# Optimization experiments

Hardware: AMD Instinct MI355X
Metric: run time of the kernel (lower is better)

The kernel has to match this reference:

```python
import jax, jax.numpy as jnp
import numpy as np

H = 4          # heads
C = 32         # out_channels per head
NEG_SLOPE = 0.2
N_NODES = 50000
N_EDGES = 600000
F_IN = 128
OUT_DIM = 10
N_GRAPHS = 32


def _gat_params(keys, f_in, scale=0.05):
    hc = H * C
    return dict(
        Wl=jax.random.normal(keys[0], (f_in, hc)) * scale,
        bl=jnp.zeros((hc,)),
        Wr=jax.random.normal(keys[1], (f_in, hc)) * scale,
        br=jnp.zeros((hc,)),
        We=jax.random.normal(keys[2], (1, hc)) * scale,   # lin_edge, bias=False in PyG
        att=jax.random.normal(keys[3], (H, C)) * scale,
        bias=jnp.zeros((hc,)),
    )


def setup_inputs() -> dict:
    key = jax.random.key(0)
    ks = jax.random.split(key, 16)
    x = jax.random.normal(ks[0], (N_NODES, F_IN), dtype=jnp.float32)
    edge_index = jax.random.randint(ks[1], (2, N_EDGES), 0, N_NODES, dtype=jnp.int32)
    edge_weight = jax.random.uniform(ks[2], (N_EDGES, 1), dtype=jnp.float32)
    batch = jnp.sort(jax.random.randint(ks[3], (N_NODES,), 0, N_GRAPHS, dtype=jnp.int32))
    p1 = _gat_params(ks[4:8], F_IN)
    p2 = _gat_params(ks[8:12], H * C)
    fc_W = jax.random.normal(ks[12], (H * C, OUT_DIM)) * 0.05
    fc_b = jnp.zeros((OUT_DIM,))
    return dict(
        x=x, edge_index=edge_index, edge_weight=edge_weight, batch=batch,
        p1_Wl=p1['Wl'], p1_bl=p1['bl'], p1_Wr=p1['Wr'], p1_br=p1['br'],
        p1_We=p1['We'], p1_att=p1['att'], p1_bias=p1['bias'],
        p2_Wl=p2['Wl'], p2_bl=p2['bl'], p2_Wr=p2['Wr'], p2_br=p2['br'],
        p2_We=p2['We'], p2_att=p2['att'], p2_bias=p2['bias'],
        fc_W=fc_W, fc_b=fc_b,
    )


def _add_self_loops(src, dst, eattr, n):
    # PyG fill_value='mean': self-loop attr = mean of incoming edge_attr per node
    loop = jnp.arange(n, dtype=src.dtype)
    cnt = jax.ops.segment_sum(jnp.ones((src.shape[0],), eattr.dtype), dst, num_segments=n)
    loop_attr = jax.ops.segment_sum(eattr, dst, num_segments=n) / jnp.maximum(cnt, 1.0)[:, None]
    return (jnp.concatenate([src, loop]), jnp.concatenate([dst, loop]),
            jnp.concatenate([eattr, loop_attr], axis=0))


def _gatv2_conv(x, src, dst, eattr, Wl, bl, Wr, br, We, att, bias, n):
    x_l = (x @ Wl + bl).reshape(n, H, C)   # source transform
    x_r = (x @ Wr + br).reshape(n, H, C)   # target transform
    e_feat = (eattr @ We).reshape(-1, H, C)
    # per-edge message [E2, H, C]
    m = jax.nn.leaky_relu(x_l[src] + x_r[dst] + e_feat, NEG_SLOPE)
    alpha = jnp.einsum('ehc,hc->eh', m, att)            # [E2, H]
    amax = jax.ops.segment_max(alpha, dst, num_segments=n)
    amax = jnp.where(jnp.isfinite(amax), amax, 0.0)
    ex = jnp.exp(alpha - amax[dst])
    denom = jax.ops.segment_sum(ex, dst, num_segments=n)
    a = ex / (denom[dst] + 1e-16)                       # segment softmax
    out = jax.ops.segment_sum(a[:, :, None] * x_l[src], dst, num_segments=n)
    return out.reshape(n, H * C) + bias


def reference(x, edge_index, edge_weight, batch,
              p1_Wl, p1_bl, p1_Wr, p1_br, p1_We, p1_att, p1_bias,
              p2_Wl, p2_bl, p2_Wr, p2_br, p2_We, p2_att, p2_bias,
              fc_W, fc_b):
    n = x.shape[0]
    src, dst, eattr = _add_self_loops(edge_index[0], edge_index[1], edge_weight, n)
    h = _gatv2_conv(x, src, dst, eattr, p1_Wl, p1_bl, p1_Wr, p1_br, p1_We, p1_att, p1_bias, n)
    h = _gatv2_conv(h, src, dst, eattr, p2_Wl, p2_bl, p2_Wr, p2_br, p2_We, p2_att, p2_bias, n)
    cnt = jax.ops.segment_sum(jnp.ones((n,), h.dtype), batch, num_segments=N_GRAPHS)
    pooled = jax.ops.segment_sum(h, batch, num_segments=N_GRAPHS) / jnp.maximum(cnt, 1.0)[:, None]
    out = pooled @ fc_W + fc_b
    return out, pooled
```

## Files before the change

kernel.cpp:

```cpp
#include <hip/hip_runtime.h>
#include <hip/hip_bf16.h>
#include <cstdint>

static inline int cdiv(int a, int b){ return (a + b - 1) / b; }

typedef __attribute__((ext_vector_type(8))) short short8v;
typedef __attribute__((ext_vector_type(4))) float float4v;
typedef __attribute__((ext_vector_type(2))) float f2;

#define ELLW 48

__device__ inline float bf2f(unsigned short u){ return __uint_as_float(((unsigned)u) << 16); }
__device__ inline unsigned short f2bf(float f){
  unsigned u = __float_as_uint(f);
  u += 0x7fffu + ((u >> 16) & 1u);
  return (unsigned short)(u >> 16);
}
__device__ inline float4 ldbf4(const unsigned short* p){
  ushort4 u = *(const ushort4*)p;
  return make_float4(bf2f(u.x), bf2f(u.y), bf2f(u.z), bf2f(u.w));
}
__device__ inline f2 lo2(float4 v){ f2 r; r.x = v.x; r.y = v.y; return r; }
__device__ inline f2 hi2(float4 v){ f2 r; r.x = v.z; r.y = v.w; return r; }
__device__ inline int sniff16(const unsigned* __restrict__ xw){
  int good = 0;
  #pragma unroll
  for (int j = 0; j < 16; ++j){
    float v = __uint_as_float(xw[j] << 16);
    float a = fabsf(v);
    good += (v == 0.f) || (a >= 6.1e-5f && a <= 64.f);
  }
  return good > 8;
}

struct P16 { const void* p[16]; };
__global__ void k_prep(P16 s, const unsigned* __restrict__ xw,
                       unsigned long long* __restrict__ deg64, float* __restrict__ pool,
                       int pz, int N,
                       unsigned short* __restrict__ Wf, unsigned short* __restrict__ bb,
                       unsigned short* __restrict__ sm){
  int i = blockIdx.x * blockDim.x + threadIdx.x;
  if (i < N) deg64[i] = 0ull;
  if (i < pz) pool[i] = 0.f;
  if (i >= 68106) return;
  const int bf = sniff16(xw);
  auto rd = [&](const void* q, int j) -> unsigned short {
    return bf ? ((const unsigned short*)q)[j] : f2bf(((const float*)q)[j]);
  };
  if (i < 65536){
    int l = i >> 15, r = i & 32767;
    int j = r & 7, n = (r >> 3) & 255, kq = r >> 11;
    int k = kq * 8 + j;
    const void* W = (n < 128) ? (l ? s.p[7] : s.p[0]) : (l ? s.p[9] : s.p[2]);
    Wf[i] = rd(W, k * 128 + (n & 127));
  } else if (i < 66048){
    int i2 = i - 65536;
    int l = i2 >> 8, n = i2 & 255;
    const void* b = (n < 128) ? (l ? s.p[8] : s.p[1]) : (l ? s.p[10] : s.p[3]);
    bb[i2] = rd(b, n & 127);
  } else {
    int j = i - 66048;
    const void* q; int o;
    if      (j < 128){ q = s.p[4];  o = j; }
    else if (j < 256){ q = s.p[5];  o = j - 128; }
    else if (j < 384){ q = s.p[6];  o = j - 256; }
    else if (j < 512){ q = s.p[11]; o = j - 384; }
    else if (j < 640){ q = s.p[12]; o = j - 512; }
    else if (j < 768){ q = s.p[13]; o = j - 640; }
    else if (j < 2048){ q = s.p[14]; o = j - 768; }
    else { q = s.p[15]; o = j - 2048; }
    sm[j] = rd(q, o);
  }
}

__global__ __launch_bounds__(256)
void k_esc(const int* __restrict__ ei, const void* __restrict__ ew,
           const unsigned* __restrict__ xw,
           unsigned long long* __restrict__ deg64, unsigned* __restrict__ eE,
           int E, int P, int N){
  const int bf = sniff16(xw);
  const int part = blockIdx.x & 7;
  const int lo = part * P;
  const int hi = min(lo + P, N);
  const int base = (int)(blockIdx.x >> 3) * 2048;
  const int end = min(base + 2048, E);
  for (int e = base + (int)threadIdx.x; e < end; e += 256){
    int dst = ei[E + e];
    if (dst < lo || dst >= hi) continue;
    int src = ei[e];
    unsigned short w16; float w;
    if (bf){ w16 = ((const unsigned short*)ew)[e]; w = bf2f(w16); }
    else   { w = ((const float*)ew)[e]; w16 = f2bf(w); }
    unsigned long long pk = (1ull << 40) + (unsigned long long)(unsigned)(w * 1048576.0f + 0.5f);
    unsigned long long old = atomicAdd(&deg64[dst], pk);
    int pos = min((int)(old >> 40), ELLW - 1);
    eE[dst * ELLW + pos] = (unsigned)src | ((unsigned)w16 << 16);
  }
}

template<bool ACT_BF_FIXED>
__global__ __launch_bounds__(256)
void k_gemm2(const void* __restrict__ actv, const unsigned* __restrict__ xw,
             const unsigned short* __restrict__ Wf, const unsigned short* __restrict__ bb,
             unsigned short* __restrict__ outL, unsigned short* __restrict__ outR, int nrows){
  __shared__ unsigned short As[64][136];
  __shared__ unsigned short Cs[4][64][40];
  const int abf = ACT_BF_FIXED ? 1 : sniff16(xw);
  const int t = threadIdx.x;
  const int row0 = blockIdx.x * 64;
  for (int c = t; c < 2048; c += 256){
    int row = c >> 5, col4 = (c & 31) * 4;
    int r = row0 + row;
    ushort4 v = make_ushort4(0, 0, 0, 0);
    if (r < nrows){
      if (abf) v = *(const ushort4*)((const unsigned short*)actv + (size_t)r * 128 + col4);
      else {
        float4 f = *(const float4*)((const float*)actv + (size_t)r * 128 + col4);
        v.x = f2bf(f.x); v.y = f2bf(f.y); v.z = f2bf(f.z); v.w = f2bf(f.w);
      }
    }
    *(ushort4*)&As[row][col4] = v;
  }
  __syncthreads();
  const int wv = t >> 6, lane = t & 63;
  const int l15 = lane & 15, q = lane >> 4;
  #pragma unroll
  for (int half = 0; half < 2; ++half){
    const int ntb = wv * 4 + half * 2;
    short8v bfr[2][4];
    #pragma unroll
    for (int nt = 0; nt < 2; ++nt){
      int n = (ntb + nt) * 16 + l15;
      #pragma unroll
      for (int ks = 0; ks < 4; ++ks)
        bfr[nt][ks] = *(const short8v*)(Wf + ((((ks * 4 + q) * 256 + n)) << 3));
    }
    float4v acc[4][2];
    #pragma unroll
    for (int mi = 0; mi < 4; ++mi)
      #pragma unroll
      for (int nt = 0; nt < 2; ++nt)
        acc[mi][nt] = (float4v){0.f, 0.f, 0.f, 0.f};
    #pragma unroll
    for (int mi = 0; mi < 4; ++mi){
      short8v afr[4];
      #pragma unroll
      for (int ks = 0; ks < 4; ++ks)
        afr[ks] = *(const short8v*)&As[mi * 16 + l15][ks * 32 + q * 8];
      #pragma unroll
      for (int nt = 0; nt < 2; ++nt)
        #pragma unroll
        for (int ks = 0; ks < 4; ++ks)
          acc[mi][nt] = __builtin_amdgcn_mfma_f32_16x16x32_bf16(afr[ks], bfr[nt][ks], acc[mi][nt], 0, 0, 0);
    }
    #pragma unroll
    for (int nt = 0; nt < 2; ++nt){
      int n = (ntb + nt) * 16 + l15;
      float bias = bf2f(bb[n]);
      #pragma unroll
      for (int mi = 0; mi < 4; ++mi)
        #pragma unroll
        for (int rr = 0; rr < 4; ++rr)
          Cs[wv][mi * 16 + q * 4 + rr][nt * 16 + l15] = f2bf(acc[mi][nt][rr] + bias);
    }
    const int gb = wv * 64 + half * 32;
    unsigned short* outp = (gb < 128) ? outL : outR;
    const int gcol = gb & 127;
    #pragma unroll
    for (int k = 0; k < 4; ++k){
      int q2 = lane + 64 * k;
      int row = q2 >> 2, gc = q2 & 3;
      int grow = row0 + row;
      if (grow < nrows){
        uint4 v = *(const uint4*)&Cs[wv][row][gc * 8];
        *(uint4*)(outp + (size_t)grow * 128 + gcol + gc * 8) = v;
      }
    }
  }
}

__global__ __launch_bounds__(256)
void k_node(const unsigned short* __restrict__ A, const unsigned short* __restrict__ B,
            const unsigned long long* __restrict__ deg64, const unsigned* __restrict__ eE,
            const unsigned short* __restrict__ We, const unsigned short* __restrict__ att,
            const unsigned short* __restrict__ bias, unsigned short* __restrict__ H, int N){
  int node = (blockIdx.x * 256 + threadIdx.x) >> 5;
  if (node >= N) return;
  int lane = threadIdx.x & 31;
  unsigned long long v64 = deg64[node];
  int d = (int)(v64 >> 40);
  float ws = (float)(v64 & 0xFFFFFFFFFFull) * (1.0f / 1048576.0f);
  float lw = ws / fmaxf((float)d, 1.0f);
  int dc = min(d, ELLW);
  const unsigned* eb = eE + (size_t)node * ELLW;
  float4 xrv = ldbf4(B + (size_t)node * 128 + lane * 4);
  float4 wev = ldbf4(We + lane * 4);
  float4 atv = ldbf4(att + lane * 4);
  f2 xr01 = lo2(xrv), xr23 = hi2(xrv);
  f2 we01 = lo2(wev), we23 = hi2(wev);
  f2 at01 = lo2(atv), at23 = hi2(atv);
  float4 xlsv = ldbf4(A + (size_t)node * 128 + lane * 4);
  f2 xls01 = lo2(xlsv), xls23 = hi2(xlsv);
  f2 t01 = lw * we01 + (xls01 + xr01);
  f2 t23 = lw * we23 + (xls23 + xr23);
  f2 m01 = __builtin_elementwise_max(t01, 0.2f * t01);
  f2 m23 = __builtin_elementwise_max(t23, 0.2f * t23);
  f2 pv = m01 * at01 + m23 * at23;
  float s = pv.x + pv.y;
  s += __shfl_xor(s, 1);
  s += __shfl_xor(s, 2);
  s += __shfl_xor(s, 4);
  float exs = __expf(fminf(s, 60.f));
  float denom = exs;
  f2 acc01 = exs * xls01;
  f2 acc23 = exs * xls23;
  const int last = dc - 1;
  const int nI = (dc + 3) >> 2;
  auto ldev = [&](int g) -> uint4 {
    int p = g * 4;
    if (p + 4 <= dc) return *(const uint4*)(eb + p);
    uint4 e;
    e.x = eb[p];
    e.y = eb[min(p + 1, last)];
    e.z = eb[min(p + 2, last)];
    e.w = eb[min(p + 3, last)];
    return e;
  };
  uint4 evc = make_uint4(0, 0, 0, 0), evn = make_uint4(0, 0, 0, 0);
  ushort4 rc0, rc1, rc2, rc3;
  if (nI > 0){
    evc = ldev(0);
    rc0 = *(const ushort4*)(A + (size_t)(evc.x & 0xffff) * 128 + lane * 4);
    rc1 = *(const ushort4*)(A + (size_t)(evc.y & 0xffff) * 128 + lane * 4);
    rc2 = *(const ushort4*)(A + (size_t)(evc.z & 0xffff) * 128 + lane * 4);
    rc3 = *(const ushort4*)(A + (size_t)(evc.w & 0xffff) * 128 + lane * 4);
    if (nI > 1) evn = ldev(1);
  }
  #pragma unroll 1
  for (int g = 0; g < nI; ++g){
    ushort4 rn0, rn1, rn2, rn3;
    uint4 evn2 = make_uint4(0, 0, 0, 0);
    if (g + 1 < nI){
      rn0 = *(const ushort4*)(A + (size_t)(evn.x & 0xffff) * 128 + lane * 4);
      rn1 = *(const ushort4*)(A + (size_t)(evn.y & 0xffff) * 128 + lane * 4);
      rn2 = *(const ushort4*)(A + (size_t)(evn.z & 0xffff) * 128 + lane * 4);
      rn3 = *(const ushort4*)(A + (size_t)(evn.w & 0xffff) * 128 + lane * 4);
    }
    if (g + 2 < nI) evn2 = ldev(g + 2);
    const int p = g * 4;
    float w0 = bf2f((unsigned short)(evc.x >> 16));
    float w1 = bf2f((unsigned short)(evc.y >> 16));
    float w2 = bf2f((unsigned short)(evc.z >> 16));
    float w3 = bf2f((unsigned short)(evc.w >> 16));
    float4 x0 = make_float4(bf2f(rc0.x), bf2f(rc0.y), bf2f(rc0.z), bf2f(rc0.w));
    float4 x1 = make_float4(bf2f(rc1.x), bf2f(rc1.y), bf2f(rc1.z), bf2f(rc1.w));
    float4 x2 = make_float4(bf2f(rc2.x), bf2f(rc2.y), bf2f(rc2.z), bf2f(rc2.w));
    float4 x3 = make_float4(bf2f(rc3.x), bf2f(rc3.y), bf2f(rc3.z), bf2f(rc3.w));
    f2 x0l = lo2(x0), x0h = hi2(x0);
    f2 x1l = lo2(x1), x1h = hi2(x1);
    f2 x2l = lo2(x2), x2h = hi2(x2);
    f2 x3l = lo2(x3), x3h = hi2(x3);
    f2 a01, a23, b01, b23;
    float s0, s1, s2, s3;
    a01 = w0 * we01 + (x0l + xr01);
    a23 = w0 * we23 + (x0h + xr23);
    a01 = __builtin_elementwise_max(a01, 0.2f * a01);
    a23 = __builtin_elementwise_max(a23, 0.2f * a23);
    b01 = a01 * at01 + a23 * at23;  s0 = b01.x + b01.y;
    a01 = w1 * we01 + (x1l + xr01);
    a23 = w1 * we23 + (x1h + xr23);
    a01 = __builtin_elementwise_max(a01, 0.2f * a01);
    a23 = __builtin_elementwise_max(a23, 0.2f * a23);
    b23 = a01 * at01 + a23 * at23;  s1 = b23.x + b23.y;
    a01 = w2 * we01 + (x2l + xr01);
    a23 = w2 * we23 + (x2h + xr23);
    a01 = __builtin_elementwise_max(a01, 0.2f * a01);
    a23 = __builtin_elementwise_max(a23, 0.2f * a23);
    b01 = a01 * at01 + a23 * at23;  s2 = b01.x + b01.y;
    a01 = w3 * we01 + (x3l + xr01);
    a23 = w3 * we23 + (x3h + xr23);
    a01 = __builtin_elementwise_max(a01, 0.2f * a01);
    a23 = __builtin_elementwise_max(a23, 0.2f * a23);
    b23 = a01 * at01 + a23 * at23;  s3 = b23.x + b23.y;
    s0 += __shfl_xor(s0, 1); s1 += __shfl_xor(s1, 1); s2 += __shfl_xor(s2, 1); s3 += __shfl_xor(s3, 1);
    s0 += __shfl_xor(s0, 2); s1 += __shfl_xor(s1, 2); s2 += __shfl_xor(s2, 2); s3 += __shfl_xor(s3, 2);
    s0 += __shfl_xor(s0, 4); s1 += __shfl_xor(s1, 4); s2 += __shfl_xor(s2, 4); s3 += __shfl_xor(s3, 4);
    float ex0 = __expf(fminf(s0, 60.f));
    float ex1 = __expf(fminf(s1, 60.f));
    float ex2 = __expf(fminf(s2, 60.f));
    float ex3 = __expf(fminf(s3, 60.f));
    if (p + 1 >= dc) ex1 = 0.f;
    if (p + 2 >= dc) ex2 = 0.f;
    if (p + 3 >= dc) ex3 = 0.f;
    denom += (ex0 + ex1) + (ex2 + ex3);
    acc01 = ex0 * x0l + acc01;  acc23 = ex0 * x0h + acc23;
    acc01 = ex1 * x1l + acc01;  acc23 = ex1 * x1h + acc23;
    acc01 = ex2 * x2l + acc01;  acc23 = ex2 * x2h + acc23;
    acc01 = ex3 * x3l + acc01;  acc23 = ex3 * x3h + acc23;
    if (g + 1 < nI){
      evc = evn; evn = evn2;
      rc0 = rn0; rc1 = rn1; rc2 = rn2; rc3 = rn3;
    }
  }
  float inv = 1.f / (denom + 1e-16f);
  float4 bv = ldbf4(bias + lane * 4);
  ushort4 o;
  o.x = f2bf(fmaf(acc01.x, inv, bv.x));
  o.y = f2bf(fmaf(acc01.y, inv, bv.y));
  o.z = f2bf(fmaf(acc23.x, inv, bv.z));
  o.w = f2bf(fmaf(acc23.y, inv, bv.w));
  *(ushort4*)(H + (size_t)node * 128 + lane * 4) = o;
}

__global__ __launch_bounds__(256)
void k_pool(const unsigned short* __restrict__ Cb, const int* __restrict__ batch,
            float* __restrict__ pool, float* __restrict__ gcnt, int N){
  __shared__ float sp[4][128];
  __shared__ float scnt[4];
  const int t = threadIdx.x;
  const int lane = t & 31, grp = t >> 5;
  const int r0 = blockIdx.x * 64;
  const int r1 = min(r0 + 64, N);
  if (r0 >= N) return;
  const int gmin = batch[r0];
  const int gmax = batch[r1 - 1];
  const int ngr = gmax - gmin + 1;
  const bool fits = (ngr <= 4);
  if (t < 4) scnt[t] = 0.f;
  for (int i = t; i < 4 * 128; i += 256) ((float*)sp)[i] = 0.f;
  __syncthreads();
  int curg = -1; float4 s = make_float4(0.f, 0.f, 0.f, 0.f); float cnt = 0.f;
  for (int r = r0 + grp; r < r1; r += 8){
    int g = batch[r];
    if (g != curg){
      if (curg >= 0){
        if (fits){
          float* pp = sp[curg - gmin] + lane * 4;
          atomicAdd(pp + 0, s.x); atomicAdd(pp + 1, s.y);
          atomicAdd(pp + 2, s.z); atomicAdd(pp + 3, s.w);
          if (lane == 0) atomicAdd(&scnt[curg - gmin], cnt);
        } else {
          float* pp = pool + (size_t)curg * 128 + lane * 4;
          atomicAdd(pp + 0, s.x); atomicAdd(pp + 1, s.y);
          atomicAdd(pp + 2, s.z); atomicAdd(pp + 3, s.w);
          if (lane == 0) atomicAdd(&gcnt[curg], cnt);
        }
      }
      s = make_float4(0.f, 0.f, 0.f, 0.f); cnt = 0.f; curg = g;
    }
    float4 v = ldbf4(Cb + (size_t)r * 128 + lane * 4);
    s.x += v.x; s.y += v.y; s.z += v.z; s.w += v.w;
    cnt += 1.f;
  }
  if (curg >= 0){
    if (fits){
      float* pp = sp[curg - gmin] + lane * 4;
      atomicAdd(pp + 0, s.x); atomicAdd(pp + 1, s.y);
      atomicAdd(pp + 2, s.z); atomicAdd(pp + 3, s.w);
      if (lane == 0) atomicAdd(&scnt[curg - gmin], cnt);
    } else {
      float* pp = pool + (size_t)curg * 128 + lane * 4;
      atomicAdd(pp + 0, s.x); atomicAdd(pp + 1, s.y);
      atomicAdd(pp + 2, s.z); atomicAdd(pp + 3, s.w);
      if (lane == 0) atomicAdd(&gcnt[curg], cnt);
    }
  }
  __syncthreads();
  if (fits){
    for (int i = t; i < ngr * 128; i += 256){
      int gg = i >> 7;
      atomicAdd(&pool[(size_t)(gmin + gg) * 128 + (i & 127)], ((float*)sp)[i]);
    }
    if (t < ngr) atomicAdd(&gcnt[gmin + t], scnt[t]);
  }
}

__global__ __launch_bounds__(256)
void k_fc(const float* __restrict__ pool, const float* __restrict__ gcnt,
          const unsigned short* __restrict__ fcW, const unsigned short* __restrict__ fcb,
          const unsigned* __restrict__ xw, void* __restrict__ outv, int G){
  __shared__ float sp[32 * 128];
  int t = threadIdx.x;
  int bf = sniff16(xw);
  unsigned short* ob = (unsigned short*)outv;
  float* of = (float*)outv;
  for (int idx = t; idx < G * 128; idx += 256){
    int g = idx >> 7;
    float p = pool[idx] / fmaxf(gcnt[g], 1.0f);
    sp[idx] = p;
    if (bf) ob[G * 10 + idx] = f2bf(p); else of[G * 10 + idx] = p;
  }
  __syncthreads();
  for (int idx = t; idx < G * 10; idx += 256){
    int g = idx / 10, o = idx - g * 10;
    float acc = bf2f(fcb[o]);
    const float* sg = sp + g * 128;
    #pragma unroll 4
    for (int c = 0; c < 128; ++c) acc = fmaf(sg[c], bf2f(fcW[c * 10 + o]), acc);
    if (bf) ob[idx] = f2bf(acc); else of[idx] = acc;
  }
}

extern "C" void kernel_launch(void* const* d_in, const int* in_sizes, int n_in,
                              void* d_out, int out_size, void* d_ws, size_t ws_size,
                              hipStream_t stream){
  const void* x    = d_in[0];
  const unsigned* xw = (const unsigned*)d_in[0];
  const int* ei    = (const int*)d_in[1];
  const void* ew   = d_in[2];
  const int* batch = (const int*)d_in[3];

  const int N  = in_sizes[3];
  const int E  = in_sizes[2];
  const int G  = out_size / 138;

  char* w = (char*)d_ws;
  auto take = [&](size_t nbytes) -> char* {
    char* p = w; w += (nbytes + 255) & ~(size_t)255; return p;
  };
  unsigned short* Abf  = (unsigned short*)take((size_t)N * 128 * 2);
  unsigned short* Bbf  = (unsigned short*)take((size_t)N * 128 * 2);
  unsigned short* Hb   = (unsigned short*)take((size_t)N * 128 * 2);
  unsigned long long* deg64 = (unsigned long long*)take((size_t)N * 8);
  unsigned* eE     = (unsigned*)take((size_t)N * ELLW * 4);
  float*    pool   = (float*)take((size_t)(G * 128 + G) * 4);
  float*    gcnt   = pool + (size_t)G * 128;
  unsigned short* Wf = (unsigned short*)take((size_t)2 * 32768 * 2);
  unsigned short* bb = (unsigned short*)take(512 * 2);
  unsigned short* sm = (unsigned short*)take(2058 * 2);

  P16 ps;
  for (int i = 0; i < 16; ++i) ps.p[i] = d_in[4 + i];
  const unsigned short* p1We = sm + 0;
  const unsigned short* p1at = sm + 128;
  const unsigned short* p1bs = sm + 256;
  const unsigned short* p2We = sm + 384;
  const unsigned short* p2at = sm + 512;
  const unsigned short* p2bs = sm + 640;
  const unsigned short* fcW  = sm + 768;
  const unsigned short* fcb  = sm + 2048;

  const int prepT = (68106 > N) ? 68106 : N;
  k_prep<<<cdiv(prepT, 256), 256, 0, stream>>>(ps, xw, deg64, pool, G * 128 + G, N, Wf, bb, sm);

  const int P = cdiv(N, 8);
  k_esc<<<cdiv(E, 2048) * 8, 256, 0, stream>>>(ei, ew, xw, deg64, eE, E, P, N);

  k_gemm2<false><<<cdiv(N, 64), 256, 0, stream>>>(x, xw, Wf, bb, Abf, Bbf, N);
  k_node<<<cdiv(N, 8), 256, 0, stream>>>(Abf, Bbf, deg64, eE, p1We, p1at, p1bs, Hb, N);

  k_gemm2<true><<<cdiv(N, 64), 256, 0, stream>>>(Hb, xw, Wf + 32768, bb + 256, Abf, Bbf, N);
  k_node<<<cdiv(N, 8), 256, 0, stream>>>(Abf, Bbf, deg64, eE, p2We, p2at, p2bs, Hb, N);

  k_pool<<<cdiv(N, 64), 256, 0, stream>>>(Hb, batch, pool, gcnt, N);
  k_fc<<<1, 256, 0, stream>>>(pool, gcnt, fcW, fcb, xw, d_out, G);
}
```

Baseline: 274.9 us.

## Split node edges across half-warps with 16B gathers; replicate pool accumulators

The per-node aggregation kernel now has each 32-lane group split into two half-warps. Each lane handles 8 channels with 16-byte bf16 loads, and the two halves process alternate edges in parallel. Their partial softmax sums and accumulators are merged with a cross-half shuffle at the end. This halves the dependent edge iterations per node and widens the gather loads, but it drops the deeper software prefetch of neighbour rows. Separately, the pooling kernel spreads its atomics over 8 replicated accumulator copies to reduce contention, and the final FC kernel sums those copies back together.

```diff
diff --git a/kernel.cpp b/kernel.cpp
--- a/kernel.cpp
+++ b/kernel.cpp
@@ -9,6 +9,8 @@
 typedef __attribute__((ext_vector_type(2))) float f2;
 
 #define ELLW 48
+#define PREP 8
+#define PRSTR 4224
 
 __device__ inline float bf2f(unsigned short u){ return __uint_as_float(((unsigned)u) << 16); }
 __device__ inline unsigned short f2bf(float f){
@@ -20,8 +22,17 @@
   ushort4 u = *(const ushort4*)p;
   return make_float4(bf2f(u.x), bf2f(u.y), bf2f(u.z), bf2f(u.w));
 }
-__device__ inline f2 lo2(float4 v){ f2 r; r.x = v.x; r.y = v.y; return r; }
-__device__ inline f2 hi2(float4 v){ f2 r; r.x = v.z; r.y = v.w; return r; }
+__device__ inline f2 lrelu2(f2 a){ return __builtin_elementwise_max(a, 0.2f * a); }
+struct f8 { f2 a, b, c, d; };
+__device__ inline f8 ld8(const unsigned short* p){
+  uint4 u = *(const uint4*)p;
+  f8 r;
+  r.a.x = __uint_as_float(u.x << 16); r.a.y = __uint_as_float(u.x & 0xffff0000u);
+  r.b.x = __uint_as_float(u.y << 16); r.b.y = __uint_as_float(u.y & 0xffff0000u);
+  r.c.x = __uint_as_float(u.z << 16); r.c.y = __uint_as_float(u.z & 0xffff0000u);
+  r.d.x = __uint_as_float(u.w << 16); r.d.y = __uint_as_float(u.w & 0xffff0000u);
+  return r;
+}
 __device__ inline int sniff16(const unsigned* __restrict__ xw){
   int good = 0;
   #pragma unroll
@@ -184,38 +195,43 @@
             const unsigned long long* __restrict__ deg64, const unsigned* __restrict__ eE,
             const unsigned short* __restrict__ We, const unsigned short* __restrict__ att,
             const unsigned short* __restrict__ bias, unsigned short* __restrict__ H, int N){
-  int node = (blockIdx.x * 256 + threadIdx.x) >> 5;
+  const int node = (blockIdx.x * 256 + threadIdx.x) >> 5;
   if (node >= N) return;
-  int lane = threadIdx.x & 31;
+  const int lane = threadIdx.x & 31;
+  const int ln = lane & 15;
+  const int hi = lane >> 4;
+  const int cb = ln * 8;
   unsigned long long v64 = deg64[node];
   int d = (int)(v64 >> 40);
   float ws = (float)(v64 & 0xFFFFFFFFFFull) * (1.0f / 1048576.0f);
   float lw = ws / fmaxf((float)d, 1.0f);
   int dc = min(d, ELLW);
   const unsigned* eb = eE + (size_t)node * ELLW;
-  float4 xrv = ldbf4(B + (size_t)node * 128 + lane * 4);
-  float4 wev = ldbf4(We + lane * 4);
-  float4 atv = ldbf4(att + lane * 4);
-  f2 xr01 = lo2(xrv), xr23 = hi2(xrv);
-  f2 we01 = lo2(wev), we23 = hi2(wev);
-  f2 at01 = lo2(atv), at23 = hi2(atv);
-  float4 xlsv = ldbf4(A + (size_t)node * 128 + lane * 4);
-  f2 xls01 = lo2(xlsv), xls23 = hi2(xlsv);
-  f2 t01 = lw * we01 + (xls01 + xr01);
-  f2 t23 = lw * we23 + (xls23 + xr23);
-  f2 m01 = __builtin_elementwise_max(t01, 0.2f * t01);
-  f2 m23 = __builtin_elementwise_max(t23, 0.2f * t23);
-  f2 pv = m01 * at01 + m23 * at23;
-  float s = pv.x + pv.y;
+  f8 xr = ld8(B + (size_t)node * 128 + cb);
+  f8 we = ld8(We + cb);
+  f8 at = ld8(att + cb);
+  f8 xs = ld8(A + (size_t)node * 128 + cb);
+  {
+  }
+  f2 a0 = lw * we.a + (xs.a + xr.a);
+  f2 a1 = lw * we.b + (xs.b + xr.b);
+  f2 a2 = lw * we.c + (xs.c + xr.c);
+  f2 a3 = lw * we.d + (xs.d + xr.d);
+  a0 = lrelu2(a0); a1 = lrelu2(a1); a2 = lrelu2(a2); a3 = lrelu2(a3);
+  f2 b = a0 * at.a;
+  b = a1 * at.b + b;
+  b = a2 * at.c + b;
+  b = a3 * at.d + b;
+  float s = b.x + b.y;
   s += __shfl_xor(s, 1);
   s += __shfl_xor(s, 2);
-  s += __shfl_xor(s, 4);
   float exs = __expf(fminf(s, 60.f));
-  float denom = exs;
-  f2 acc01 = exs * xls01;
-  f2 acc23 = exs * xls23;
+  if (hi) exs = 0.f;
+  float dn = exs;
+  f8 acc;
+  acc.a = exs * xs.a; acc.b = exs * xs.b; acc.c = exs * xs.c; acc.d = exs * xs.d;
   const int last = dc - 1;
-  const int nI = (dc + 3) >> 2;
+  const int nG = (dc + 3) >> 2;
   auto ldev = [&](int g) -> uint4 {
     int p = g * 4;
     if (p + 4 <= dc) return *(const uint4*)(eb + p);
@@ -226,95 +242,76 @@
     e.w = eb[min(p + 3, last)];
     return e;
   };
-  uint4 evc = make_uint4(0, 0, 0, 0), evn = make_uint4(0, 0, 0, 0);
-  ushort4 rc0, rc1, rc2, rc3;
-  if (nI > 0){
-    evc = ldev(0);
-    rc0 = *(const ushort4*)(A + (size_t)(evc.x & 0xffff) * 128 + lane * 4);
-    rc1 = *(const ushort4*)(A + (size_t)(evc.y & 0xffff) * 128 + lane * 4);
-    rc2 = *(const ushort4*)(A + (size_t)(evc.z & 0xffff) * 128 + lane * 4);
-    rc3 = *(const ushort4*)(A + (size_t)(evc.w & 0xffff) * 128 + lane * 4);
-    if (nI > 1) evn = ldev(1);
-  }
-  #pragma unroll 1
-  for (int g = 0; g < nI; ++g){
-    ushort4 rn0, rn1, rn2, rn3;
-    uint4 evn2 = make_uint4(0, 0, 0, 0);
-    if (g + 1 < nI){
-      rn0 = *(const ushort4*)(A + (size_t)(evn.x & 0xffff) * 128 + lane * 4);
-      rn1 = *(const ushort4*)(A + (size_t)(evn.y & 0xffff) * 128 + lane * 4);
-      rn2 = *(const ushort4*)(A + (size_t)(evn.z & 0xffff) * 128 + lane * 4);
-      rn3 = *(const ushort4*)(A + (size_t)(evn.w & 0xffff) * 128 + lane * 4);
-    }
-    if (g + 2 < nI) evn2 = ldev(g + 2);
-    const int p = g * 4;
-    float w0 = bf2f((unsigned short)(evc.x >> 16));
-    float w1 = bf2f((unsigned short)(evc.y >> 16));
-    float w2 = bf2f((unsigned short)(evc.z >> 16));
-    float w3 = bf2f((unsigned short)(evc.w >> 16));
-    float4 x0 = make_float4(bf2f(rc0.x), bf2f(rc0.y), bf2f(rc0.z), bf2f(rc0.w));
-    float4 x1 = make_float4(bf2f(rc1.x), bf2f(rc1.y), bf2f(rc1.z), bf2f(rc1.w));
-    float4 x2 = make_float4(bf2f(rc2.x), bf2f(rc2.y), bf2f(rc2.z), bf2f(rc2.w));
-    float4 x3 = make_float4(bf2f(rc3.x), bf2f(rc3.y), bf2f(rc3.z), bf2f(rc3.w));
-    f2 x0l = lo2(x0), x0h = hi2(x0);
-    f2 x1l = lo2(x1), x1h = hi2(x1);
-    f2 x2l = lo2(x2), x2h = hi2(x2);
-    f2 x3l = lo2(x3), x3h = hi2(x3);
-    f2 a01, a23, b01, b23;
-    float s0, s1, s2, s3;
-    a01 = w0 * we01 + (x0l + xr01);
-    a23 = w0 * we23 + (x0h + xr23);
-    a01 = __builtin_elementwise_max(a01, 0.2f * a01);
-    a23 = __builtin_elementwise_max(a23, 0.2f * a23);
-    b01 = a01 * at01 + a23 * at23;  s0 = b01.x + b01.y;
-    a01 = w1 * we01 + (x1l + xr01);
-    a23 = w1 * we23 + (x1h + xr23);
-    a01 = __builtin_elementwise_max(a01, 0.2f * a01);
-    a23 = __builtin_elementwise_max(a23, 0.2f * a23);
-    b23 = a01 * at01 + a23 * at23;  s1 = b23.x + b23.y;
-    a01 = w2 * we01 + (x2l + xr01);
-    a23 = w2 * we23 + (x2h + xr23);
-    a01 = __builtin_elementwise_max(a01, 0.2f * a01);
-    a23 = __builtin_elementwise_max(a23, 0.2f * a23);
-    b01 = a01 * at01 + a23 * at23;  s2 = b01.x + b01.y;
-    a01 = w3 * we01 + (x3l + xr01);
-    a23 = w3 * we23 + (x3h + xr23);
-    a01 = __builtin_elementwise_max(a01, 0.2f * a01);
-    a23 = __builtin_elementwise_max(a23, 0.2f * a23);
-    b23 = a01 * at01 + a23 * at23;  s3 = b23.x + b23.y;
-    s0 += __shfl_xor(s0, 1); s1 += __shfl_xor(s1, 1); s2 += __shfl_xor(s2, 1); s3 += __shfl_xor(s3, 1);
-    s0 += __shfl_xor(s0, 2); s1 += __shfl_xor(s1, 2); s2 += __shfl_xor(s2, 2); s3 += __shfl_xor(s3, 2);
-    s0 += __shfl_xor(s0, 4); s1 += __shfl_xor(s1, 4); s2 += __shfl_xor(s2, 4); s3 += __shfl_xor(s3, 4);
-    float ex0 = __expf(fminf(s0, 60.f));
-    float ex1 = __expf(fminf(s1, 60.f));
-    float ex2 = __expf(fminf(s2, 60.f));
-    float ex3 = __expf(fminf(s3, 60.f));
-    if (p + 1 >= dc) ex1 = 0.f;
-    if (p + 2 >= dc) ex2 = 0.f;
-    if (p + 3 >= dc) ex3 = 0.f;
-    denom += (ex0 + ex1) + (ex2 + ex3);
-    acc01 = ex0 * x0l + acc01;  acc23 = ex0 * x0h + acc23;
-    acc01 = ex1 * x1l + acc01;  acc23 = ex1 * x1h + acc23;
-    acc01 = ex2 * x2l + acc01;  acc23 = ex2 * x2h + acc23;
-    acc01 = ex3 * x3l + acc01;  acc23 = ex3 * x3h + acc23;
-    if (g + 1 < nI){
-      evc = evn; evn = evn2;
-      rc0 = rn0; rc1 = rn1; rc2 = rn2; rc3 = rn3;
-    }
-  }
-  float inv = 1.f / (denom + 1e-16f);
-  float4 bv = ldbf4(bias + lane * 4);
-  ushort4 o;
-  o.x = f2bf(fmaf(acc01.x, inv, bv.x));
-  o.y = f2bf(fmaf(acc01.y, inv, bv.y));
-  o.z = f2bf(fmaf(acc23.x, inv, bv.z));
-  o.w = f2bf(fmaf(acc23.y, inv, bv.w));
-  *(ushort4*)(H + (size_t)node * 128 + lane * 4) = o;
+  uint4 evc = make_uint4(0, 0, 0, 0);
+  if (nG > 0) evc = ldev(0);
+  for (int g = 0; g < nG; ++g){
+    uint4 evn = (g + 1 < nG) ? ldev(g + 1) : evc;
+    const unsigned e0 = hi ? evc.y : evc.x;
+    const unsigned e1 = hi ? evc.w : evc.z;
+    f8 x0 = ld8(A + (size_t)(e0 & 0xffff) * 128 + cb);
+    f8 x1 = ld8(A + (size_t)(e1 & 0xffff) * 128 + cb);
+    {
+      float ww = bf2f((unsigned short)(e0 >> 16));
+      f2 c0 = ww * we.a + (x0.a + xr.a);
+      f2 c1 = ww * we.b + (x0.b + xr.b);
+      f2 c2 = ww * we.c + (x0.c + xr.c);
+      f2 c3 = ww * we.d + (x0.d + xr.d);
+      c0 = lrelu2(c0); c1 = lrelu2(c1); c2 = lrelu2(c2); c3 = lrelu2(c3);
+      f2 bb2 = c0 * at.a;
+      bb2 = c1 * at.b + bb2;
+      bb2 = c2 * at.c + bb2;
+      bb2 = c3 * at.d + bb2;
+      float sl = bb2.x + bb2.y;
+      sl += __shfl_xor(sl, 1);
+      sl += __shfl_xor(sl, 2);
+      float ex = __expf(fminf(sl, 60.f));
+      if (g * 4 + hi >= dc) ex = 0.f;
+      dn += ex;
+      acc.a = ex * x0.a + acc.a; acc.b = ex * x0.b + acc.b;
+      acc.c = ex * x0.c + acc.c; acc.d = ex * x0.d + acc.d;
+    }
+    {
+      float ww = bf2f((unsigned short)(e1 >> 16));
+      f2 c0 = ww * we.a + (x1.a + xr.a);
+      f2 c1 = ww * we.b + (x1.b + xr.b);
+      f2 c2 = ww * we.c + (x1.c + xr.c);
+      f2 c3 = ww * we.d + (x1.d + xr.d);
+      c0 = lrelu2(c0); c1 = lrelu2(c1); c2 = lrelu2(c2); c3 = lrelu2(c3);
+      f2 bb2 = c0 * at.a;
+      bb2 = c1 * at.b + bb2;
+      bb2 = c2 * at.c + bb2;
+      bb2 = c3 * at.d + bb2;
+      float sl = bb2.x + bb2.y;
+      sl += __shfl_xor(sl, 1);
+      sl += __shfl_xor(sl, 2);
+      float ex = __expf(fminf(sl, 60.f));
+      if (g * 4 + 2 + hi >= dc) ex = 0.f;
+      dn += ex;
+      acc.a = ex * x1.a + acc.a; acc.b = ex * x1.b + acc.b;
+      acc.c = ex * x1.c + acc.c; acc.d = ex * x1.d + acc.d;
+    }
+    evc = evn;
+  }
+  dn += __shfl_xor(dn, 16);
+  acc.a.x += __shfl_xor(acc.a.x, 16); acc.a.y += __shfl_xor(acc.a.y, 16);
+  acc.b.x += __shfl_xor(acc.b.x, 16); acc.b.y += __shfl_xor(acc.b.y, 16);
+  acc.c.x += __shfl_xor(acc.c.x, 16); acc.c.y += __shfl_xor(acc.c.y, 16);
+  acc.d.x += __shfl_xor(acc.d.x, 16); acc.d.y += __shfl_xor(acc.d.y, 16);
+  if (hi == 0){
+    float inv = 1.f / (dn + 1e-16f);
+    f8 bv = ld8(bias + cb);
+    uint4 o;
+    o.x = (unsigned)f2bf(fmaf(acc.a.x, inv, bv.a.x)) | ((unsigned)f2bf(fmaf(acc.a.y, inv, bv.a.y)) << 16);
+    o.y = (unsigned)f2bf(fmaf(acc.b.x, inv, bv.b.x)) | ((unsigned)f2bf(fmaf(acc.b.y, inv, bv.b.y)) << 16);
+    o.z = (unsigned)f2bf(fmaf(acc.c.x, inv, bv.c.x)) | ((unsigned)f2bf(fmaf(acc.c.y, inv, bv.c.y)) << 16);
+    o.w = (unsigned)f2bf(fmaf(acc.d.x, inv, bv.d.x)) | ((unsigned)f2bf(fmaf(acc.d.y, inv, bv.d.y)) << 16);
+    *(uint4*)(H + (size_t)node * 128 + cb) = o;
+  }
 }
 
 __global__ __launch_bounds__(256)
 void k_pool(const unsigned short* __restrict__ Cb, const int* __restrict__ batch,
-            float* __restrict__ pool, float* __restrict__ gcnt, int N){
+            float* __restrict__ pool, int N){
   __shared__ float sp[4][128];
   __shared__ float scnt[4];
   const int t = threadIdx.x;
@@ -322,6 +319,7 @@
   const int r0 = blockIdx.x * 64;
   const int r1 = min(r0 + 64, N);
   if (r0 >= N) return;
+  float* pr = pool + (size_t)(blockIdx.x & (PREP - 1)) * PRSTR;
   const int gmin = batch[r0];
   const int gmax = batch[r1 - 1];
   const int ngr = gmax - gmin + 1;
@@ -340,10 +338,10 @@
           atomicAdd(pp + 2, s.z); atomicAdd(pp + 3, s.w);
           if (lane == 0) atomicAdd(&scnt[curg - gmin], cnt);
         } else {
-          float* pp = pool + (size_t)curg * 128 + lane * 4;
+          float* pp = pr + (size_t)curg * 128 + lane * 4;
           atomicAdd(pp + 0, s.x); atomicAdd(pp + 1, s.y);
           atomicAdd(pp + 2, s.z); atomicAdd(pp + 3, s.w);
-          if (lane == 0) atomicAdd(&gcnt[curg], cnt);
+          if (lane == 0) atomicAdd(&pr[4096 + curg], cnt);
         }
       }
       s = make_float4(0.f, 0.f, 0.f, 0.f); cnt = 0.f; curg = g;
@@ -359,34 +357,45 @@
       atomicAdd(pp + 2, s.z); atomicAdd(pp + 3, s.w);
       if (lane == 0) atomicAdd(&scnt[curg - gmin], cnt);
     } else {
-      float* pp = pool + (size_t)curg * 128 + lane * 4;
+      float* pp = pr + (size_t)curg * 128 + lane * 4;
       atomicAdd(pp + 0, s.x); atomicAdd(pp + 1, s.y);
       atomicAdd(pp + 2, s.z); atomicAdd(pp + 3, s.w);
-      if (lane == 0) atomicAdd(&gcnt[curg], cnt);
+      if (lane == 0) atomicAdd(&pr[4096 + curg], cnt);
     }
   }
   __syncthreads();
   if (fits){
     for (int i = t; i < ngr * 128; i += 256){
       int gg = i >> 7;
-      atomicAdd(&pool[(size_t)(gmin + gg) * 128 + (i & 127)], ((float*)sp)[i]);
-    }
-    if (t < ngr) atomicAdd(&gcnt[gmin + t], scnt[t]);
+      atomicAdd(&pr[(size_t)(gmin + gg) * 128 + (i & 127)], ((float*)sp)[i]);
+    }
+    if (t < ngr) atomicAdd(&pr[4096 + gmin + t], scnt[t]);
   }
 }
 
 __global__ __launch_bounds__(256)
-void k_fc(const float* __restrict__ pool, const float* __restrict__ gcnt,
+void k_fc(const float* __restrict__ pool,
           const unsigned short* __restrict__ fcW, const unsigned short* __restrict__ fcb,
           const unsigned* __restrict__ xw, void* __restrict__ outv, int G){
   __shared__ float sp[32 * 128];
+  __shared__ float scn[32];
   int t = threadIdx.x;
   int bf = sniff16(xw);
   unsigned short* ob = (unsigned short*)outv;
   float* of = (float*)outv;
+  if (t < G){
+    float c = 0.f;
+    #pragma unroll
+    for (int r = 0; r < PREP; ++r) c += pool[(size_t)r * PRSTR + 4096 + t];
+    scn[t] = fmaxf(c, 1.0f);
+  }
+  __syncthreads();
   for (int idx = t; idx < G * 128; idx += 256){
     int g = idx >> 7;
-    float p = pool[idx] / fmaxf(gcnt[g], 1.0f);
+    float s = 0.f;
+    #pragma unroll
+    for (int r = 0; r < PREP; ++r) s += pool[(size_t)r * PRSTR + idx];
+    float p = s / scn[g];
     sp[idx] = p;
     if (bf) ob[G * 10 + idx] = f2bf(p); else of[G * 10 + idx] = p;
   }
@@ -423,8 +432,7 @@
   unsigned short* Hb   = (unsigned short*)take((size_t)N * 128 * 2);
   unsigned long long* deg64 = (unsigned long long*)take((size_t)N * 8);
   unsigned* eE     = (unsigned*)take((size_t)N * ELLW * 4);
-  float*    pool   = (float*)take((size_t)(G * 128 + G) * 4);
-  float*    gcnt   = pool + (size_t)G * 128;
+  float*    pool   = (float*)take((size_t)PREP * PRSTR * 4);
   unsigned short* Wf = (unsigned short*)take((size_t)2 * 32768 * 2);
   unsigned short* bb = (unsigned short*)take(512 * 2);
   unsigned short* sm = (unsigned short*)take(2058 * 2);
@@ -441,7 +449,7 @@
   const unsigned short* fcb  = sm + 2048;
 
   const int prepT = (68106 > N) ? 68106 : N;
-  k_prep<<<cdiv(prepT, 256), 256, 0, stream>>>(ps, xw, deg64, pool, G * 128 + G, N, Wf, bb, sm);
+  k_prep<<<cdiv(prepT, 256), 256, 0, stream>>>(ps, xw, deg64, pool, PREP * PRSTR, N, Wf, bb, sm);
 
   const int P = cdiv(N, 8);
   k_esc<<<cdiv(E, 2048) * 8, 256, 0, stream>>>(ei, ew, xw, deg64, eE, E, P, N);
@@ -452,6 +460,6 @@
   k_gemm2<true><<<cdiv(N, 64), 256, 0, stream>>>(Hb, xw, Wf + 32768, bb + 256, Abf, Bbf, N);
   k_node<<<cdiv(N, 8), 256, 0, stream>>>(Abf, Bbf, deg64, eE, p2We, p2at, p2bs, Hb, N);
 
-  k_pool<<<cdiv(N, 64), 256, 0, stream>>>(Hb, batch, pool, gcnt, N);
-  k_fc<<<1, 256, 0, stream>>>(pool, gcnt, fcW, fcb, xw, d_out, G);
-}
+  k_pool<<<cdiv(N, 64), 256, 0, stream>>>(Hb, batch, pool, N);
+  k_fc<<<1, 256, 0, stream>>>(pool, fcW, fcb, xw, d_out, G);
+}
```

New measurement: 267.3 us. 2.8% less time.
